# Optimization experiments

Hardware: AMD Instinct MI355X
Metric: run time of the kernel (lower is better)

Reference implementation:

```python
import jax, jax.numpy as jnp
import numpy as np

B, S, DIM, H = 2, 2048, 1024, 16
DH = DIM // H            # 64
G = DH // 4              # 16 quaternion groups per head
IQ = DIM // 4            # 256
ROPE_BASE = 10000.0
SCALE = DH ** -0.5


def qlinear(x, wr, wi, wj, wk, b):
    # x: [B,S,4*IQ]; strided quaternion components, exact combo from QuaternionLinear.forward
    xr, xi, xj, xk = x[..., 0::4], x[..., 1::4], x[..., 2::4], x[..., 3::4]
    o_r = xr @ wr.T - xi @ wi.T - xj @ wj.T - xk @ wk.T
    o_i = xi @ wr.T + xr @ wi.T + xk @ wk.T - xj @ wj.T
    o_j = xj @ wr.T - xk @ wk.T + xr @ wj.T + xi @ wi.T
    o_k = xk @ wr.T + xj @ wj.T - xi @ wi.T + xr @ wk.T
    out = jnp.stack([o_r, o_i, o_j, o_k], axis=-1).reshape(x.shape[:-1] + (-1,))
    return out + b


def qrope(x):
    # x: [B,H,S,DH]; left quaternion multiply u(theta) \otimes q, axis_mode='cycle'
    b, h, s, dh = x.shape
    g = dh // 4
    xq = x.reshape(b, h, s, g, 4)
    t = jnp.arange(s, dtype=x.dtype)
    inv = 1.0 / (ROPE_BASE ** (jnp.arange(g, dtype=x.dtype) / g))
    ang = t[:, None] * inv[None, :]            # [S,G]
    cos, sin = jnp.cos(ang), jnp.sin(ang)
    gi = jnp.arange(g)
    ax_i = (gi % 3 == 0).astype(x.dtype)
    ax_j = (gi % 3 == 1).astype(x.dtype)
    ax_k = (gi % 3 == 2).astype(x.dtype)
    ur, ui, uj, uk = cos, sin * ax_i, sin * ax_j, sin * ax_k   # [S,G] broadcast over [B,H,S,G]
    xr, xi, xj, xk = xq[..., 0], xq[..., 1], xq[..., 2], xq[..., 3]
    pr = ur * xr - ui * xi - uj * xj - uk * xk
    pi = ur * xi + ui * xr + uj * xk - uk * xj
    pj = ur * xj - ui * xk + uj * xr + uk * xi
    pk = ur * xk + ui * xj - uj * xi + uk * xr
    return jnp.stack([pr, pi, pj, pk], axis=-1).reshape(b, h, s, dh)


def setup_inputs() -> dict:
    key = jax.random.key(0)
    ks = jax.random.split(key, 24)
    x = jax.random.normal(ks[0], (B, S, DIM), dtype=jnp.float32)
    # causal mask: True = masked
    mask = jnp.broadcast_to(jnp.triu(jnp.ones((S, S), dtype=bool), k=1), (B, S, S))
    inp = {"x": x, "mask": mask}
    i = 1
    for proj in ("q", "k", "v", "o"):
        for comp in ("wr", "wi", "wj", "wk"):
            inp[f"{proj}_{comp}"] = jax.random.normal(ks[i], (IQ, IQ), dtype=jnp.float32) * 0.02
            i += 1
        inp[f"{proj}_b"] = jnp.zeros((DIM,), dtype=jnp.float32)
    return inp


def reference(x, mask,
              q_wr, q_wi, q_wj, q_wk, q_b,
              k_wr, k_wi, k_wj, k_wk, k_b,
              v_wr, v_wi, v_wj, v_wk, v_b,
              o_wr, o_wi, o_wj, o_wk, o_b):
    b, s, dm = x.shape
    q = qlinear(x, q_wr, q_wi, q_wj, q_wk, q_b).reshape(b, s, H, DH).transpose(0, 2, 1, 3)
    k = qlinear(x, k_wr, k_wi, k_wj, k_wk, k_b).reshape(b, s, H, DH).transpose(0, 2, 1, 3)
    v = qlinear(x, v_wr, v_wi, v_wj, v_wk, v_b).reshape(b, s, H, DH).transpose(0, 2, 1, 3)
    q, k = qrope(q), qrope(k)
    scores = jnp.einsum('bhsd,bhtd->bhst', q, k) * SCALE
    scores = jnp.where(mask[:, None, :, :], -jnp.inf, scores)
    a = jax.nn.softmax(scores, axis=-1)
    out = jnp.einsum('bhst,bhtd->bhsd', a, v).transpose(0, 2, 1, 3).reshape(b, s, dm)
    return qlinear(out, o_wr, o_wi, o_wj, o_wk, o_b)
```

## Files before the change

### kernel.cpp

```cpp
#include <hip/hip_runtime.h>
#include <stdint.h>

typedef unsigned short u16;
typedef unsigned int   u32;

#define NB   2
#define NS   2048
#define NDIM 1024
#define NH   16
#define NDH  64
#define QSCALE 0.18033688011112042f

typedef __bf16 bf16x8 __attribute__((ext_vector_type(8)));
typedef float  f32x4  __attribute__((ext_vector_type(4)));

#define MFMA_BF16(a,b,c) __builtin_amdgcn_mfma_f32_16x16x32_bf16((a),(b),(c),0,0,0)

#define XBF_OFF   (256)
#define WD_OFF    (XBF_OFF  + 8*1024*1024)
#define BIAS_OFF  (WD_OFF   + 8*1024*1024)
#define QB_OFF    (BIAS_OFF + 16384)
#define KB_OFF    (QB_OFF   + 8*1024*1024)
#define VT_OFF    (KB_OFF   + 8*1024*1024)
#define OP_OFF    (VT_OFF   + 8*1024*1024)
#define LP_OFF    (OP_OFF   + 16*1024*1024)

__device__ __forceinline__ float bf2f(u16 h){
  union { u32 u; float f; } v; v.u = ((u32)h) << 16; return v.f;
}
__device__ __forceinline__ u16 f2bf(float f){
  union { float f; u32 u; } v; v.f = f;
  u32 r = (v.u >> 16) & 1u;
  return (u16)((v.u + 0x7fffu + r) >> 16);
}
__device__ __forceinline__ u16 f2bf_rn(float f){
  union { __bf16 h; u16 u; } v; v.h = (__bf16)f; return v.u;
}
__device__ __forceinline__ float load_val(const void* p, int i, int isbf){
  return isbf ? bf2f(((const u16*)p)[i]) : ((const float*)p)[i];
}
__device__ __forceinline__ void gl_lds16(const u16* g, u16* l){
  __builtin_amdgcn_global_load_lds(
      (__attribute__((address_space(1))) void*)(uintptr_t)g,
      (__attribute__((address_space(3))) void*)(uintptr_t)l,
      16, 0, 0);
}

struct QPtrs { const void* w[16]; const void* b[4]; };

__global__ void prep_kernel(const void* __restrict__ xin, QPtrs ptrs,
                            u16* __restrict__ xbf, u16* __restrict__ wd,
                            float* __restrict__ biasf, int* __restrict__ flag){
  __shared__ int cnt;
  if (threadIdx.x == 0) cnt = 0;
  __syncthreads();
  {
    const uint4* xv = (const uint4*)xin;
    uint4 v0 = xv[threadIdx.x * 2], v1 = xv[threadIdx.x * 2 + 1];
    const u16* hh = (const u16*)&v0;
    int ok = 0;
#pragma unroll
    for (int i = 0; i < 16; ++i){
      u16 h = (i < 8) ? hh[i] : ((const u16*)&v1)[i - 8];
      int e = (h >> 7) & 0xFF;
      if ((e > 96 && e < 158) || ((h & 0x7FFF) == 0)) ok++;
    }
    atomicAdd(&cnt, ok);
  }
  __syncthreads();
  int isbf = (cnt > 3600) ? 1 : 0;
  if (blockIdx.x == 0 && threadIdx.x == 0) *flag = isbf;

  int idx = blockIdx.x * 256 + threadIdx.x;

  if (blockIdx.x < 2048){
    int t = idx;
    if (isbf){
      ((uint4*)xbf)[t] = ((const uint4*)xin)[t];
    } else {
      const float4* f4 = (const float4*)xin;
      float4 a = f4[2*t], b = f4[2*t+1];
      ushort4 lo = { f2bf(a.x), f2bf(a.y), f2bf(a.z), f2bf(a.w) };
      ushort4 hi = { f2bf(b.x), f2bf(b.y), f2bf(b.z), f2bf(b.w) };
      ((ushort4*)xbf)[2*t]   = lo;
      ((ushort4*)xbf)[2*t+1] = hi;
    }
  }

  int n = idx & 255, m = (idx >> 8) & 255, c = (idx >> 16) & 3, p = idx >> 18;
  int src = m * 256 + n;
  float vr = load_val(ptrs.w[p*4+0], src, isbf);
  float vi = load_val(ptrs.w[p*4+1], src, isbf);
  float vj = load_val(ptrs.w[p*4+2], src, isbf);
  float vk = load_val(ptrs.w[p*4+3], src, isbf);
  float o0, o1, o2, o3;
  switch (c){
    case 0:  o0 = vr; o1 = -vi; o2 = -vj; o3 = -vk; break;
    case 1:  o0 = vi; o1 =  vr; o2 = -vj; o3 =  vk; break;
    case 2:  o0 = vj; o1 =  vi; o2 =  vr; o3 = -vk; break;
    default: o0 = vk; o1 = -vi; o2 =  vj; o3 =  vr; break;
  }
  ushort4 sv = { f2bf(o0), f2bf(o1), f2bf(o2), f2bf(o3) };
  *(ushort4*)&wd[(size_t)p * 1048576 + (size_t)(4*m + c) * 1024 + 4*n] = sv;
  if (idx < 4096){
    int pp = idx >> 10, oo = idx & 1023;
    biasf[idx] = load_val(ptrs.b[pp], oo, isbf);
  }
}

__global__ __launch_bounds__(256)
void gemm_qkv_kernel(const u16* __restrict__ A, const u16* __restrict__ Bw,
                     const float* __restrict__ bias,
                     u16* __restrict__ qb, u16* __restrict__ kb, u16* __restrict__ vt){
  __shared__ u16 sA[3][128 * 32];
  __shared__ u16 sB[3][128 * 32];
  int tid = threadIdx.x, w = tid >> 6, lane = tid & 63, quad = lane >> 4, l16 = lane & 15;

  int lid = (int)blockIdx.y * 24 + (int)blockIdx.x;
  int swz = (lid & 7) * 96 + (lid >> 3);
  int n0 = (swz % 24) * 128, m0 = (swz / 24) * 128;

  f32x4 acc[4][4];
#pragma unroll
  for (int i = 0; i < 4; ++i)
#pragma unroll
    for (int j = 0; j < 4; ++j) acc[i][j] = (f32x4){0.f, 0.f, 0.f, 0.f};

  int cp = lane & 3, rl = lane >> 2;
  int gc = (cp ^ ((rl >> 1) & 3)) * 8;
  const u16* ga = A  + (size_t)(m0 + w*16 + rl) * 1024 + gc;
  const u16* gb = Bw + (size_t)(n0 + w*16 + rl) * 1024 + gc;
  int ldo = w * 512 + lane * 8;
  int xorv = ((l16 >> 1) & 3) * 8;
  int mw = (w & 1) * 64, nw = (w >> 1) * 64;

  auto stage = [&](int k0, int b){
#pragma unroll
    for (int i = 0; i < 2; ++i){
      gl_lds16(ga + (size_t)i * 65536 + k0, &sA[b][ldo + i * 2048]);
      gl_lds16(gb + (size_t)i * 65536 + k0, &sB[b][ldo + i * 2048]);
    }
  };

  stage(0, 0);
  stage(32, 1);
  asm volatile("s_waitcnt vmcnt(4)" ::: "memory");
  __builtin_amdgcn_s_barrier();

  int bcur = 0, bnxt = 2;
  for (int it = 0; it < 32; ++it){
    if (it < 30) stage((it + 2) * 32, bnxt);
    const u16* cA = sA[bcur];
    const u16* cB = sB[bcur];
    bf16x8 af[4], bfr[4];
#pragma unroll
    for (int mt = 0; mt < 4; ++mt)
      af[mt] = *(const bf16x8*)&cA[(mw + mt*16 + l16) * 32 + (quad*8 ^ xorv)];
#pragma unroll
    for (int nt = 0; nt < 4; ++nt)
      bfr[nt] = *(const bf16x8*)&cB[(nw + nt*16 + l16) * 32 + (quad*8 ^ xorv)];
#pragma unroll
    for (int mt = 0; mt < 4; ++mt)
#pragma unroll
      for (int nt = 0; nt < 4; ++nt)
        acc[mt][nt] = MFMA_BF16(af[mt], bfr[nt], acc[mt][nt]);

    if (it < 30) asm volatile("s_waitcnt vmcnt(4)" ::: "memory");
    else         asm volatile("s_waitcnt vmcnt(0)" ::: "memory");
    __builtin_amdgcn_s_barrier();
    bcur = (bcur == 2) ? 0 : bcur + 1;
    bnxt = (bnxt == 2) ? 0 : bnxt + 1;
  }

  int proj = n0 >> 10;
  if (proj == 2){
#pragma unroll
    for (int mt = 0; mt < 4; ++mt){
      int row = m0 + mw + mt*16 + quad*4;
      int b = row >> 11, seq0 = row & 2047;
#pragma unroll
      for (int nt = 0; nt < 4; ++nt){
        int col = n0 + nw + nt*16 + l16;
        int o = col & 1023, h = o >> 6, d = o & 63;
        float bv = bias[col];
        ushort4 pv = { f2bf_rn(acc[mt][nt][0] + bv), f2bf_rn(acc[mt][nt][1] + bv),
                       f2bf_rn(acc[mt][nt][2] + bv), f2bf_rn(acc[mt][nt][3] + bv) };
        *(ushort4*)&vt[((size_t)((b*16 + h) * 64 + d)) * 2048 + seq0] = pv;
      }
    }
  } else {
    float sc = (proj == 0) ? QSCALE : 1.0f;
    u16* dst = proj ? kb : qb;
    int c = l16 & 3;
#pragma unroll
    for (int nt = 0; nt < 4; ++nt){
      int col = n0 + nw + nt*16 + l16;
      int o = col & 1023, h = o >> 6, d = o & 63;
      int g = d >> 2;
      int ax = g % 3;
      int mask = ax + 1;
      int tbl = (ax == 0) ? 0xA : (ax == 1 ? 0x6 : 0xC);
      float sgn = ((tbl >> c) & 1) ? 1.f : -1.f;
      float inv = __builtin_amdgcn_exp2f(-(float)g * 0.8304820237218405f);
      float bv = bias[col];
#pragma unroll
      for (int mt = 0; mt < 4; ++mt){
        int row0 = m0 + mw + mt*16 + quad*4;
        int b = row0 >> 11, s0 = row0 & 2047;
        size_t obase = ((size_t)((b*16 + h) * 2048 + s0)) * 64 + d;
#pragma unroll
        for (int r = 0; r < 4; ++r){
          float v = acc[mt][nt][r] + bv;
          float vp = __shfl_xor(v, mask);
          float ang = (float)(s0 + r) * inv;
          float co = __cosf(ang) * sc;
          float si = __sinf(ang) * sc * sgn;
          dst[obase + (size_t)r * 64] = f2bf_rn(co * v + si * vp);
        }
      }
    }
  }
}

__global__ __launch_bounds__(256)
void gemm_o_kernel(const u16* __restrict__ A, const u16* __restrict__ Bw,
                   const float* __restrict__ bias, void* __restrict__ dout,
                   const int* __restrict__ flag){
  __shared__ u16 sA[3][64 * 32];
  __shared__ u16 sB[3][128 * 32];
  int tid = threadIdx.x, w = tid >> 6, lane = tid & 63, quad = lane >> 4, l16 = lane & 15;
  int n0 = blockIdx.x * 128, m0 = blockIdx.y * 64;

  f32x4 acc[2][4];
#pragma unroll
  for (int i = 0; i < 2; ++i)
#pragma unroll
    for (int j = 0; j < 4; ++j) acc[i][j] = (f32x4){0.f, 0.f, 0.f, 0.f};

  int cp = lane & 3, rl = lane >> 2;
  int gc = (cp ^ ((rl >> 1) & 3)) * 8;
  int xorv = ((l16 >> 1) & 3) * 8;
  int mw = (w & 1) * 32, nw = (w >> 1) * 64;

  auto stage = [&](int k0, int b){
#pragma unroll
    for (int i = 0; i < 3; ++i){
      int ch = w * 3 + i;
      int lr = (ch < 4 ? ch : ch - 4) * 16 + rl;
      int eo = (ch < 4 ? ch : ch - 4) * 512 + lane * 8;
      if (ch < 4) gl_lds16(A  + (size_t)(m0 + lr) * 1024 + k0 + gc, &sA[b][eo]);
      else        gl_lds16(Bw + (size_t)(n0 + lr) * 1024 + k0 + gc, &sB[b][eo]);
    }
  };

  stage(0, 0);
  stage(32, 1);
  asm volatile("s_waitcnt vmcnt(3)" ::: "memory");
  __builtin_amdgcn_s_barrier();

  int bcur = 0, bnxt = 2;
  for (int it = 0; it < 32; ++it){
    if (it < 30) stage((it + 2) * 32, bnxt);
    const u16* cA = sA[bcur];
    const u16* cB = sB[bcur];
    bf16x8 af[2], bfr[4];
#pragma unroll
    for (int mt = 0; mt < 2; ++mt)
      af[mt] = *(const bf16x8*)&cA[(mw + mt*16 + l16) * 32 + (quad*8 ^ xorv)];
#pragma unroll
    for (int nt = 0; nt < 4; ++nt)
      bfr[nt] = *(const bf16x8*)&cB[(nw + nt*16 + l16) * 32 + (quad*8 ^ xorv)];
#pragma unroll
    for (int mt = 0; mt < 2; ++mt)
#pragma unroll
      for (int nt = 0; nt < 4; ++nt)
        acc[mt][nt] = MFMA_BF16(af[mt], bfr[nt], acc[mt][nt]);

    if (it < 30) asm volatile("s_waitcnt vmcnt(3)" ::: "memory");
    else         asm volatile("s_waitcnt vmcnt(0)" ::: "memory");
    __builtin_amdgcn_s_barrier();
    bcur = (bcur == 2) ? 0 : bcur + 1;
    bnxt = (bnxt == 2) ? 0 : bnxt + 1;
  }

  int isbf = *flag;
#pragma unroll
  for (int mt = 0; mt < 2; ++mt){
    int row = m0 + mw + mt*16 + quad*4;
#pragma unroll
    for (int nt = 0; nt < 4; ++nt){
      int col = n0 + nw + nt*16 + l16;
      float bv = bias[col];
#pragma unroll
      for (int r = 0; r < 4; ++r){
        float val = acc[mt][nt][r] + bv;
        size_t addr = (size_t)(row + r) * 1024 + col;
        if (isbf) ((u16*)dout)[addr] = f2bf(val);
        else      ((float*)dout)[addr] = val;
      }
    }
  }
}

#define SPT 20

__global__ __launch_bounds__(128, 2)
void attn_kernel(const u16* __restrict__ Q, const u16* __restrict__ K,
                 const u16* __restrict__ Vt, u16* __restrict__ OP,
                 float* __restrict__ LP){
  __shared__ u16 sK[2][4096];
  __shared__ u16 sPT[2][64 * SPT];
  int bh  = blockIdx.x;
  int spl = blockIdx.y;
  int z   = blockIdx.z;
  int tid = threadIdx.x, w = tid >> 6, lane = tid & 63, quad = lane >> 4, l16 = lane & 15;
  size_t kbase = (size_t)bh * 2048 * 64;
  size_t vbase = (size_t)bh * 64 * 2048;
  u16* spw = &sPT[w][0];

  auto stage = [&](int kt, int b){
    int kcol = kt * 64;
#pragma unroll
    for (int p = 0; p < 4; ++p){
      int sb = (w*4 + p) * 64;
      int slot = sb + lane;
      int row = slot >> 3, dc = (slot & 7) ^ (row & 7);
      gl_lds16(K + kbase + (size_t)(kcol + row) * 64 + dc*8, &sK[b][sb * 8]);
    }
  };

  for (int item = 0; item < 2; ++item){
    int s2 = item ? z : 31 - z;
    int rowbase = s2 * 64 + w * 32;

    bf16x8 qf[2][2];
#pragma unroll
    for (int g = 0; g < 2; ++g)
#pragma unroll
      for (int kc = 0; kc < 2; ++kc)
        qf[g][kc] = *(const bf16x8*)(Q + kbase + (size_t)(rowbase + g*16 + l16) * 64 + kc*32 + quad*8);

    f32x4 oaccT[2][4];
    float lsum[2][4];
#pragma unroll
    for (int g = 0; g < 2; ++g)
#pragma unroll
      for (int i = 0; i < 4; ++i){ oaccT[g][i] = (f32x4){0.f,0.f,0.f,0.f}; lsum[g][i] = 0.f; }

    int c = (s2 + 2) >> 1;
    int kt0 = spl ? c : 0;
    int ntiles = spl ? (s2 + 1 - c) : c;

    stage(kt0, 0);
    for (int i = 0; i < ntiles; ++i){
      int kcol = (kt0 + i) * 64;
      __syncthreads();
      if (i + 1 < ntiles) stage(kt0 + i + 1, (i + 1) & 1);
      const u16* bK = sK[i & 1];

      if (kcol <= rowbase + 31){
        bf16x8 vf[4][2];
#pragma unroll
        for (int dn = 0; dn < 4; ++dn)
#pragma unroll
          for (int kc = 0; kc < 2; ++kc)
            vf[dn][kc] = *(const bf16x8*)(Vt + vbase + (size_t)(dn*16 + l16) * 2048
                                          + kcol + kc*32 + quad*8);
        bf16x8 bk[2][4];
#pragma unroll
        for (int kc = 0; kc < 2; ++kc)
#pragma unroll
          for (int nt = 0; nt < 4; ++nt){
            int rw = nt*16 + l16;
            int ch = ((kc*4 + quad) ^ (rw & 7)) * 8;
            bk[kc][nt] = *(const bf16x8*)&bK[rw*64 + ch];
          }
#pragma unroll
        for (int g = 0; g < 2; ++g){
          int G0 = rowbase + g*16;
          if (kcol <= G0 + 15){
            f32x4 sacc[4];
#pragma unroll
            for (int nt = 0; nt < 4; ++nt) sacc[nt] = (f32x4){0.f,0.f,0.f,0.f};
#pragma unroll
            for (int kc = 0; kc < 2; ++kc)
#pragma unroll
              for (int nt = 0; nt < 4; ++nt)
                sacc[nt] = MFMA_BF16(qf[g][kc], bk[kc][nt], sacc[nt]);

            if (kcol + 63 > G0){
#pragma unroll
              for (int nt = 0; nt < 4; ++nt){
                int col = kcol + nt*16 + l16;
                ushort4 pv;
#pragma unroll
                for (int r = 0; r < 4; ++r){
                  int row = G0 + quad*4 + r;
                  float pp = (col <= row) ? __builtin_amdgcn_exp2f(sacc[nt][r]) : 0.f;
                  lsum[g][r] += pp;
                  ((u16*)&pv)[r] = f2bf_rn(pp);
                }
                *(ushort4*)&spw[(nt*16 + l16) * SPT + quad*4] = pv;
              }
            } else {
#pragma unroll
              for (int nt = 0; nt < 4; ++nt){
                ushort4 pv;
#pragma unroll
                for (int r = 0; r < 4; ++r){
                  float pp = __builtin_amdgcn_exp2f(sacc[nt][r]);
                  lsum[g][r] += pp;
                  ((u16*)&pv)[r] = f2bf_rn(pp);
                }
                *(ushort4*)&spw[(nt*16 + l16) * SPT + quad*4] = pv;
              }
            }
#pragma unroll
            for (int kc = 0; kc < 2; ++kc){
              bf16x8 pf;
#pragma unroll
              for (int j = 0; j < 8; ++j)
                pf[j] = ((const __bf16*)spw)[(kc*32 + quad*8 + j) * SPT + l16];
#pragma unroll
              for (int dn = 0; dn < 4; ++dn)
                oaccT[g][dn] = MFMA_BF16(vf[dn][kc], pf, oaccT[g][dn]);
            }
          }
        }
      }
    }

    float* scr = (float*)spw;
#pragma unroll
    for (int g = 0; g < 2; ++g)
#pragma unroll
      for (int r = 0; r < 4; ++r){
        float l = lsum[g][r];
        l += __shfl_xor(l, 1); l += __shfl_xor(l, 2);
        l += __shfl_xor(l, 4); l += __shfl_xor(l, 8);
        if (l16 == 0) scr[g*16 + quad*4 + r] = l;
      }
    float lrow[2];
#pragma unroll
    for (int g = 0; g < 2; ++g) lrow[g] = scr[g*16 + l16];

    size_t obase = ((size_t)(spl*32 + bh)) * 2048;
#pragma unroll
    for (int g = 0; g < 2; ++g){
      int row = rowbase + g*16 + l16;
      if (quad == 0) LP[obase + row] = lrow[g];
#pragma unroll
      for (int dn = 0; dn < 4; ++dn){
        ushort4 ov = { f2bf_rn(oaccT[g][dn][0]), f2bf_rn(oaccT[g][dn][1]),
                       f2bf_rn(oaccT[g][dn][2]), f2bf_rn(oaccT[g][dn][3]) };
        *(ushort4*)&OP[(obase + row) * 64 + dn*16 + quad*4] = ov;
      }
    }

    __syncthreads();
  }
}

__global__ void combine_kernel(const u16* __restrict__ OP, const float* __restrict__ LP,
                               u16* __restrict__ Ab){
  int idx = blockIdx.x * 256 + threadIdx.x;
  int dc = idx & 7, s = (idx >> 3) & 2047, bh = idx >> 14;
  size_t r0 = (size_t)bh * 2048 + s, r1 = (size_t)(32 + bh) * 2048 + s;
  float invl = 1.f / (LP[r0] + LP[r1]);
  union { uint4 v; u16 h[8]; } a0, a1; ushort4 o[2];
  a0.v = *(const uint4*)&OP[r0 * 64 + dc*8];
  a1.v = *(const uint4*)&OP[r1 * 64 + dc*8];
#pragma unroll
  for (int p = 0; p < 2; ++p)
#pragma unroll
    for (int j = 0; j < 4; ++j)
      ((u16*)&o[p])[j] = f2bf((bf2f(a0.h[p*4+j]) + bf2f(a1.h[p*4+j])) * invl);
  int b = bh >> 4, h = bh & 15;
  u16* dst = &Ab[((size_t)(b*2048 + s)) * 1024 + h*64 + dc*8];
  *(ushort4*)dst = o[0];
  *(ushort4*)(dst + 4) = o[1];
}

extern "C" void kernel_launch(void* const* d_in, const int* in_sizes, int n_in,
                              void* d_out, int out_size, void* d_ws, size_t ws_size,
                              hipStream_t stream){
  (void)in_sizes; (void)n_in; (void)out_size; (void)ws_size;
  char* ws = (char*)d_ws;
  int*   flag  = (int*)ws;
  u16*   Xbf   = (u16*)(ws + XBF_OFF);
  u16*   Wd    = (u16*)(ws + WD_OFF);
  float* biasf = (float*)(ws + BIAS_OFF);
  u16*   Qb    = (u16*)(ws + QB_OFF);
  u16*   Kb    = (u16*)(ws + KB_OFF);
  u16*   Vt    = (u16*)(ws + VT_OFF);
  u16*   OP    = (u16*)(ws + OP_OFF);
  float* LP    = (float*)(ws + LP_OFF);
  u16*   Ab    = Xbf;

  QPtrs ptrs;
  for (int p = 0; p < 4; ++p){
    for (int wi = 0; wi < 4; ++wi) ptrs.w[p*4 + wi] = d_in[2 + p*5 + wi];
    ptrs.b[p] = d_in[2 + p*5 + 4];
  }

  prep_kernel<<<4096, 256, 0, stream>>>(d_in[0], ptrs, Xbf, Wd, biasf, flag);
  gemm_qkv_kernel<<<dim3(24, 32), 256, 0, stream>>>(Xbf, Wd, biasf, Qb, Kb, Vt);
  attn_kernel<<<dim3(32, 2, 16), 128, 0, stream>>>(Qb, Kb, Vt, OP, LP);
  combine_kernel<<<2048, 256, 0, stream>>>(OP, LP, Ab);
  gemm_o_kernel<<<dim3(8, 64), 256, 0, stream>>>(Ab, Wd + 3*1048576, biasf + 3072,
                                                 d_out, flag);
}
```

Baseline: 244.3 us.

## Split prep work across blocks, double-buffer P per group, remap attention block ids

```diff
diff --git a/kernel.cpp b/kernel.cpp
--- a/kernel.cpp
+++ b/kernel.cpp
@@ -85,26 +85,27 @@
       ((ushort4*)xbf)[2*t]   = lo;
       ((ushort4*)xbf)[2*t+1] = hi;
     }
-  }
-
-  int n = idx & 255, m = (idx >> 8) & 255, c = (idx >> 16) & 3, p = idx >> 18;
-  int src = m * 256 + n;
-  float vr = load_val(ptrs.w[p*4+0], src, isbf);
-  float vi = load_val(ptrs.w[p*4+1], src, isbf);
-  float vj = load_val(ptrs.w[p*4+2], src, isbf);
-  float vk = load_val(ptrs.w[p*4+3], src, isbf);
-  float o0, o1, o2, o3;
-  switch (c){
-    case 0:  o0 = vr; o1 = -vi; o2 = -vj; o3 = -vk; break;
-    case 1:  o0 = vi; o1 =  vr; o2 = -vj; o3 =  vk; break;
-    case 2:  o0 = vj; o1 =  vi; o2 =  vr; o3 = -vk; break;
-    default: o0 = vk; o1 = -vi; o2 =  vj; o3 =  vr; break;
-  }
-  ushort4 sv = { f2bf(o0), f2bf(o1), f2bf(o2), f2bf(o3) };
-  *(ushort4*)&wd[(size_t)p * 1048576 + (size_t)(4*m + c) * 1024 + 4*n] = sv;
-  if (idx < 4096){
-    int pp = idx >> 10, oo = idx & 1023;
-    biasf[idx] = load_val(ptrs.b[pp], oo, isbf);
+  } else {
+    int wi = idx - 2048 * 256;
+    int n = wi & 255, m = (wi >> 8) & 255, p = wi >> 16;
+    int src = m * 256 + n;
+    float vr = load_val(ptrs.w[p*4+0], src, isbf);
+    float vi = load_val(ptrs.w[p*4+1], src, isbf);
+    float vj = load_val(ptrs.w[p*4+2], src, isbf);
+    float vk = load_val(ptrs.w[p*4+3], src, isbf);
+    ushort4 s0 = { f2bf(vr), f2bf(-vi), f2bf(-vj), f2bf(-vk) };
+    ushort4 s1 = { f2bf(vi), f2bf(vr),  f2bf(-vj), f2bf(vk)  };
+    ushort4 s2 = { f2bf(vj), f2bf(vi),  f2bf(vr),  f2bf(-vk) };
+    ushort4 s3 = { f2bf(vk), f2bf(-vi), f2bf(vj),  f2bf(vr)  };
+    u16* base = &wd[(size_t)p * 1048576 + (size_t)(4*m) * 1024 + 4*n];
+    *(ushort4*)(base)        = s0;
+    *(ushort4*)(base + 1024) = s1;
+    *(ushort4*)(base + 2048) = s2;
+    *(ushort4*)(base + 3072) = s3;
+    if (wi < 4096){
+      int pp = wi >> 10, oo = wi & 1023;
+      biasf[wi] = load_val(ptrs.b[pp], oo, isbf);
+    }
   }
 }
 
@@ -309,14 +310,14 @@
                  const u16* __restrict__ Vt, u16* __restrict__ OP,
                  float* __restrict__ LP){
   __shared__ u16 sK[2][4096];
-  __shared__ u16 sPT[2][64 * SPT];
-  int bh  = blockIdx.x;
-  int spl = blockIdx.y;
-  int z   = blockIdx.z;
+  __shared__ u16 sPT[2][2][64 * SPT];
+  int lid = (int)blockIdx.x + 32 * (int)blockIdx.y + 64 * (int)blockIdx.z;
+  int bh  = (lid & 7) * 4 + ((lid >> 3) & 3);
+  int spl = (lid >> 5) & 1;
+  int z   = lid >> 6;
   int tid = threadIdx.x, w = tid >> 6, lane = tid & 63, quad = lane >> 4, l16 = lane & 15;
   size_t kbase = (size_t)bh * 2048 * 64;
   size_t vbase = (size_t)bh * 64 * 2048;
-  u16* spw = &sPT[w][0];
 
   auto stage = [&](int kt, int b){
     int kcol = kt * 64;
@@ -379,6 +380,7 @@
         for (int g = 0; g < 2; ++g){
           int G0 = rowbase + g*16;
           if (kcol <= G0 + 15){
+            u16* spg = &sPT[w][g][0];
             f32x4 sacc[4];
 #pragma unroll
             for (int nt = 0; nt < 4; ++nt) sacc[nt] = (f32x4){0.f,0.f,0.f,0.f};
@@ -400,7 +402,7 @@
                   lsum[g][r] += pp;
                   ((u16*)&pv)[r] = f2bf_rn(pp);
                 }
-                *(ushort4*)&spw[(nt*16 + l16) * SPT + quad*4] = pv;
+                *(ushort4*)&spg[(nt*16 + l16) * SPT + quad*4] = pv;
               }
             } else {
 #pragma unroll
@@ -412,7 +414,7 @@
                   lsum[g][r] += pp;
                   ((u16*)&pv)[r] = f2bf_rn(pp);
                 }
-                *(ushort4*)&spw[(nt*16 + l16) * SPT + quad*4] = pv;
+                *(ushort4*)&spg[(nt*16 + l16) * SPT + quad*4] = pv;
               }
             }
 #pragma unroll
@@ -420,7 +422,7 @@
               bf16x8 pf;
 #pragma unroll
               for (int j = 0; j < 8; ++j)
-                pf[j] = ((const __bf16*)spw)[(kc*32 + quad*8 + j) * SPT + l16];
+                pf[j] = ((const __bf16*)spg)[(kc*32 + quad*8 + j) * SPT + l16];
 #pragma unroll
               for (int dn = 0; dn < 4; ++dn)
                 oaccT[g][dn] = MFMA_BF16(vf[dn][kc], pf, oaccT[g][dn]);
@@ -430,7 +432,7 @@
       }
     }
 
-    float* scr = (float*)spw;
+    float* scr = (float*)&sPT[w][0][0];
 #pragma unroll
     for (int g = 0; g < 2; ++g)
 #pragma unroll
@@ -503,7 +505,7 @@
     ptrs.b[p] = d_in[2 + p*5 + 4];
   }
 
-  prep_kernel<<<4096, 256, 0, stream>>>(d_in[0], ptrs, Xbf, Wd, biasf, flag);
+  prep_kernel<<<3072, 256, 0, stream>>>(d_in[0], ptrs, Xbf, Wd, biasf, flag);
   gemm_qkv_kernel<<<dim3(24, 32), 256, 0, stream>>>(Xbf, Wd, biasf, Qb, Kb, Vt);
   attn_kernel<<<dim3(32, 2, 16), 128, 0, stream>>>(Qb, Kb, Vt, OP, LP);
   combine_kernel<<<2048, 256, 0, stream>>>(OP, LP, Ab);
```

After: 238.1 us. -2.6%, faster.
